# Kernel tuning notes

Hardware: AMD Instinct MI355X
Metric: run time of the kernel (lower is better)

## Reference

```python
import jax, jax.numpy as jnp
import numpy as np

N, D, H, L = 50000, 64, 4, 3
HD = D // H
E = 800000
EPS = 1e-5


def _layernorm(x, g, b):
    m = x.mean(-1, keepdims=True)
    v = ((x - m) ** 2).mean(-1, keepdims=True)
    return (x - m) * jax.lax.rsqrt(v + EPS) * g + b


def setup_inputs() -> dict:
    key = jax.random.key(0)
    ks = jax.random.split(key, 24)
    s = 0.05
    inp = {
        'feats': jax.random.normal(ks[0], (N, D), jnp.float32),
        'edge_index': jax.random.randint(ks[1], (2, E), 0, N, jnp.int64),
        'edge_attr': jax.random.uniform(ks[2], (E,), jnp.float32),
    }
    names = ['Wq', 'Wk', 'Wv', 'Wo', 'W1', 'W2']
    for i, n in enumerate(names):
        inp[n] = jax.random.normal(ks[3 + i], (L, D, D), jnp.float32) * s
    bnames = ['bq', 'bk', 'bv', 'bo', 'b1', 'b2']
    for i, n in enumerate(bnames):
        inp[n] = jnp.zeros((L, D), jnp.float32)
    inp['g1'] = jnp.ones((L, D), jnp.float32)
    inp['be1'] = jnp.zeros((L, D), jnp.float32)
    inp['g2'] = jnp.ones((L, D), jnp.float32)
    inp['be2'] = jnp.zeros((L, D), jnp.float32)
    return inp


def reference(feats, edge_index, edge_attr, Wq, bq, Wk, bk, Wv, bv, Wo, bo,
              W1, b1, W2, b2, g1, be1, g2, be2):
    row, col = edge_index[0], edge_index[1]  # source, destination nodes
    inv_sqrt = 1.0 / np.sqrt(HD).astype(np.float32)
    outs = []
    for l in range(L):
        # multi-head edge-indexed dot-product attention
        q = (feats @ Wq[l] + bq[l]).reshape(N, H, HD)
        k = (feats @ Wk[l] + bk[l]).reshape(N, H, HD)
        v = (feats @ Wv[l] + bv[l]).reshape(N, H, HD)
        scores = (q[col] * k[row]).sum(-1) * inv_sqrt       # [E, H]
        scores = scores * edge_attr[:, None]                # mult_attr modulation
        smax = jax.ops.segment_max(scores, col, num_segments=N)
        alpha = jnp.exp(scores - smax[col])
        denom = jax.ops.segment_sum(alpha, col, num_segments=N)
        alpha = alpha / denom[col]                          # scatter softmax
        agg = jax.ops.segment_sum(alpha[:, :, None] * v[row], col, num_segments=N)
        att = agg.reshape(N, D) @ Wo[l] + bo[l]
        feats = _layernorm(feats + att, g1[l], be1[l])      # res1 + norm1
        mlp = jax.nn.relu(feats @ W1[l] + b1[l]) @ W2[l] + b2[l]
        feats = _layernorm(feats + mlp, g2[l], be2[l])      # res2 + norm2
        outs.append(feats)
    return jnp.stack(outs)  # [L, N, D]
```

## Files before the change

kernel.cpp:

```cpp
#include <hip/hip_runtime.h>

#define NN 50000
#define DIM 64
#define NHEAD 4
#define NEDGE 800000
#define NLAYER 3
#define LN_EPS 1e-5f
#define SCAN_BLOCKS ((NN + 255) / 256)
#define ROWS 8

__device__ __forceinline__ float bcast(float x, int l) {
    return __uint_as_float(__builtin_amdgcn_readlane(__float_as_uint(x), l));
}

__device__ __forceinline__ unsigned int bf16rtn(float x) {
    unsigned int u = __float_as_uint(x);
    return (u + 0x7FFFu + ((u >> 16) & 1u)) >> 16;
}
__device__ __forceinline__ float blo(unsigned int u) {
    return __uint_as_float(u << 16);
}
__device__ __forceinline__ float bhi(unsigned int u) {
    return __uint_as_float(u & 0xFFFF0000u);
}


__global__ __launch_bounds__(256) void zero_kernel(int* __restrict__ p, int n) {
    int i = blockIdx.x * blockDim.x + threadIdx.x;
    if (i < n) p[i] = 0;
}

__global__ __launch_bounds__(256) void deg_kernel(const int* __restrict__ ei,
                                                  int* __restrict__ deg) {
    int e = blockIdx.x * blockDim.x + threadIdx.x;
    if (e < NEDGE) atomicAdd(&deg[ei[NEDGE + e]], 1);
}

__global__ __launch_bounds__(256) void scan1_kernel(const int* __restrict__ deg,
                                                    int* __restrict__ tmp,
                                                    int* __restrict__ bsum) {
    __shared__ int s[256];
    int t = threadIdx.x;
    int i = blockIdx.x * 256 + t;
    int v = (i < NN) ? deg[i] : 0;
    s[t] = v;
    __syncthreads();
    for (int off = 1; off < 256; off <<= 1) {
        int x = (t >= off) ? s[t - off] : 0;
        __syncthreads();
        s[t] += x;
        __syncthreads();
    }
    if (i < NN) tmp[i] = s[t] - v;
    if (t == 255) bsum[blockIdx.x] = s[255];
}

__global__ __launch_bounds__(256) void scan2_kernel(int* __restrict__ bsum) {
    __shared__ int s[256];
    int t = threadIdx.x;
    int v = (t < SCAN_BLOCKS) ? bsum[t] : 0;
    s[t] = v;
    __syncthreads();
    for (int off = 1; off < 256; off <<= 1) {
        int x = (t >= off) ? s[t - off] : 0;
        __syncthreads();
        s[t] += x;
        __syncthreads();
    }
    if (t < SCAN_BLOCKS) bsum[t] = s[t] - v;
}

__global__ __launch_bounds__(256) void scan3_kernel(const int* __restrict__ tmp,
                                                    const int* __restrict__ bsum,
                                                    int* __restrict__ rowptr,
                                                    int* __restrict__ cursor) {
    int i = blockIdx.x * 256 + threadIdx.x;
    if (i < NN) {
        int v = tmp[i] + bsum[i >> 8];
        rowptr[i] = v;
        cursor[i] = v;
    }
    if (i == 0) rowptr[NN] = NEDGE;
}

__global__ __launch_bounds__(256) void fill_kernel(const int* __restrict__ ei,
                                                   const float* __restrict__ attr,
                                                   int* __restrict__ cursor,
                                                   int2* __restrict__ csr) {
    int e = blockIdx.x * blockDim.x + threadIdx.x;
    if (e >= NEDGE) return;
    int src = ei[e];
    int dst = ei[NEDGE + e];
    int idx = atomicAdd(&cursor[dst], 1);
    int2 pk;
    pk.x = src;
    pk.y = __float_as_int(attr[e]);
    csr[idx] = pk;
}


__global__ __launch_bounds__(256) void qkv_kernel(
    const float* __restrict__ feats,
    const float* __restrict__ Wq, const float* __restrict__ Wk, const float* __restrict__ Wv,
    const float* __restrict__ bq, const float* __restrict__ bk, const float* __restrict__ bv,
    float* __restrict__ q, unsigned int* __restrict__ kpk, unsigned int* __restrict__ vpk) {
    int wave = threadIdx.x >> 6;
    int lane = threadIdx.x & 63;
    int n0 = (blockIdx.x * 4 + wave) * ROWS;

    const float* rowp[ROWS];
    float qa[ROWS], ka[ROWS], va[ROWS];
    float biq = bq[lane], bik = bk[lane], biv = bv[lane];
    #pragma unroll
    for (int r = 0; r < ROWS; ++r) {
        int nu = __builtin_amdgcn_readfirstlane(min(n0 + r, NN - 1));
        rowp[r] = feats + (size_t)nu * DIM;
        qa[r] = biq; ka[r] = bik; va[r] = biv;
    }
    #pragma unroll
    for (int kk = 0; kk < DIM; ++kk) {
        float wq = Wq[kk * DIM + lane];
        float wk = Wk[kk * DIM + lane];
        float wv = Wv[kk * DIM + lane];
        #pragma unroll
        for (int r = 0; r < ROWS; ++r) {
            float x = rowp[r][kk];
            qa[r] = fmaf(x, wq, qa[r]);
            ka[r] = fmaf(x, wk, ka[r]);
            va[r] = fmaf(x, wv, va[r]);
        }
    }
    bool evenLane = (lane & 1) == 0;
    #pragma unroll
    for (int r = 0; r < ROWS; ++r) {
        int n = n0 + r;
        if (n < NN) q[n * DIM + lane] = qa[r] * 0.25f;
        unsigned int bk_ = bf16rtn(ka[r]);
        unsigned int bv_ = bf16rtn(va[r]);
        unsigned int nk = __shfl_xor(bk_, 1, 64);
        unsigned int nv = __shfl_xor(bv_, 1, 64);
        if (n < NN && evenLane) {
            kpk[n * 32 + (lane >> 1)] = bk_ | (nk << 16);
            vpk[n * 32 + (lane >> 1)] = bv_ | (nv << 16);
        }
    }
}

__global__ __launch_bounds__(256) void attn_kernel(
    const int* __restrict__ rowptr, const int2* __restrict__ csr,
    const float* __restrict__ q,
    const unsigned int* __restrict__ kpk, const unsigned int* __restrict__ vpk,
    float* __restrict__ agg) {
    int wave = threadIdx.x >> 6;
    int lane = threadIdx.x & 63;
    int quarter = lane >> 4;
    int slot = (lane >> 3) & 1;
    int g = lane & 7;
    int n = blockIdx.x * 16 + wave * 4 + quarter;
    if (n >= NN) return;

    float4 qa = *(const float4*)&q[n * DIM + 8 * g];
    float4 qb = *(const float4*)&q[n * DIM + 8 * g + 4];
    int beg = rowptr[n], end = rowptr[n + 1];

    float denom = 0.f;
    float a0 = 0.f, a1 = 0.f, a2 = 0.f, a3 = 0.f;
    float a4 = 0.f, a5 = 0.f, a6 = 0.f, a7 = 0.f;

    for (int ii = beg + slot; ii < end; ii += 2) {
        int2 me = csr[ii];
        int src = me.x;
        float at = __int_as_float(me.y);
        uint4 ku = *(const uint4*)&kpk[src * 32 + 4 * g];
        uint4 vu = *(const uint4*)&vpk[src * 32 + 4 * g];
        float p = qa.x * blo(ku.x);
        p = fmaf(qa.y, bhi(ku.x), p);
        p = fmaf(qa.z, blo(ku.y), p);
        p = fmaf(qa.w, bhi(ku.y), p);
        p = fmaf(qb.x, blo(ku.z), p);
        p = fmaf(qb.y, bhi(ku.z), p);
        p = fmaf(qb.z, blo(ku.w), p);
        p = fmaf(qb.w, bhi(ku.w), p);
        p += __shfl_xor(p, 1, 64);
        float w = __expf(p * at);
        denom += w;
        a0 = fmaf(w, blo(vu.x), a0);
        a1 = fmaf(w, bhi(vu.x), a1);
        a2 = fmaf(w, blo(vu.y), a2);
        a3 = fmaf(w, bhi(vu.y), a3);
        a4 = fmaf(w, blo(vu.z), a4);
        a5 = fmaf(w, bhi(vu.z), a5);
        a6 = fmaf(w, blo(vu.w), a6);
        a7 = fmaf(w, bhi(vu.w), a7);
    }
    denom += __shfl_xor(denom, 8, 64);
    a0 += __shfl_xor(a0, 8, 64);
    a1 += __shfl_xor(a1, 8, 64);
    a2 += __shfl_xor(a2, 8, 64);
    a3 += __shfl_xor(a3, 8, 64);
    a4 += __shfl_xor(a4, 8, 64);
    a5 += __shfl_xor(a5, 8, 64);
    a6 += __shfl_xor(a6, 8, 64);
    a7 += __shfl_xor(a7, 8, 64);

    if (slot == 0) {
        float inv = (denom > 0.f) ? 1.f / denom : 0.f;
        float4 o1; o1.x = a0 * inv; o1.y = a1 * inv; o1.z = a2 * inv; o1.w = a3 * inv;
        float4 o2; o2.x = a4 * inv; o2.y = a5 * inv; o2.z = a6 * inv; o2.w = a7 * inv;
        *(float4*)&agg[n * DIM + 8 * g] = o1;
        *(float4*)&agg[n * DIM + 8 * g + 4] = o2;
    }
}

__global__ __launch_bounds__(256) void post_kernel(
    const float* __restrict__ feats_in,
    const float* __restrict__ agg,
    const float* __restrict__ Wo, const float* __restrict__ bo,
    const float* __restrict__ W1, const float* __restrict__ b1,
    const float* __restrict__ W2, const float* __restrict__ b2,
    const float* __restrict__ g1, const float* __restrict__ be1,
    const float* __restrict__ g2, const float* __restrict__ be2,
    float* __restrict__ out) {
    int wave = threadIdx.x >> 6;
    int lane = threadIdx.x & 63;
    int n0 = (blockIdx.x * 4 + wave) * ROWS;

    float acc[ROWS], xin[ROWS];
    float bio = bo[lane];
    #pragma unroll
    for (int r = 0; r < ROWS; ++r) {
        int n = min(n0 + r, NN - 1);
        xin[r] = agg[n * DIM + lane];
        acc[r] = bio;
    }
    #pragma unroll
    for (int kk = 0; kk < DIM; ++kk) {
        float w = Wo[kk * DIM + lane];
        #pragma unroll
        for (int r = 0; r < ROWS; ++r)
            acc[r] = fmaf(bcast(xin[r], kk), w, acc[r]);
    }
    float gg1 = g1[lane], bb1 = be1[lane];
    #pragma unroll
    for (int r = 0; r < ROWS; ++r) {
        int n = min(n0 + r, NN - 1);
        float x = feats_in[n * DIM + lane] + acc[r];
        float s1 = x, s2 = x * x;
        #pragma unroll
        for (int o = 32; o >= 1; o >>= 1) {
            s1 += __shfl_xor(s1, o, 64);
            s2 += __shfl_xor(s2, o, 64);
        }
        float mean = s1 * (1.f / 64.f);
        float var = fmaf(-mean, mean, s2 * (1.f / 64.f));
        xin[r] = (x - mean) * rsqrtf(var + LN_EPS) * gg1 + bb1;
    }
    float bi1 = b1[lane];
    #pragma unroll
    for (int r = 0; r < ROWS; ++r) acc[r] = bi1;
    #pragma unroll
    for (int kk = 0; kk < DIM; ++kk) {
        float w = W1[kk * DIM + lane];
        #pragma unroll
        for (int r = 0; r < ROWS; ++r)
            acc[r] = fmaf(bcast(xin[r], kk), w, acc[r]);
    }
    float h[ROWS];
    #pragma unroll
    for (int r = 0; r < ROWS; ++r) h[r] = fmaxf(acc[r], 0.f);
    float bi2 = b2[lane];
    #pragma unroll
    for (int r = 0; r < ROWS; ++r) acc[r] = bi2;
    #pragma unroll
    for (int kk = 0; kk < DIM; ++kk) {
        float w = W2[kk * DIM + lane];
        #pragma unroll
        for (int r = 0; r < ROWS; ++r)
            acc[r] = fmaf(bcast(h[r], kk), w, acc[r]);
    }
    float gg2 = g2[lane], bb2 = be2[lane];
    #pragma unroll
    for (int r = 0; r < ROWS; ++r) {
        int n = n0 + r;
        float x2 = xin[r] + acc[r];
        float s1 = x2, s2 = x2 * x2;
        #pragma unroll
        for (int o = 32; o >= 1; o >>= 1) {
            s1 += __shfl_xor(s1, o, 64);
            s2 += __shfl_xor(s2, o, 64);
        }
        float mean = s1 * (1.f / 64.f);
        float var = fmaf(-mean, mean, s2 * (1.f / 64.f));
        if (n < NN)
            out[n * DIM + lane] = (x2 - mean) * rsqrtf(var + LN_EPS) * gg2 + bb2;
    }
}

extern "C" void kernel_launch(void* const* d_in, const int* in_sizes, int n_in,
                              void* d_out, int out_size, void* d_ws, size_t ws_size,
                              hipStream_t stream) {
    const float* feats = (const float*)d_in[0];
    const int*   ei    = (const int*)d_in[1];
    const float* attr  = (const float*)d_in[2];
    const float* Wq = (const float*)d_in[3];
    const float* Wk = (const float*)d_in[4];
    const float* Wv = (const float*)d_in[5];
    const float* Wo = (const float*)d_in[6];
    const float* W1 = (const float*)d_in[7];
    const float* W2 = (const float*)d_in[8];
    const float* bq = (const float*)d_in[9];
    const float* bk = (const float*)d_in[10];
    const float* bv = (const float*)d_in[11];
    const float* bo = (const float*)d_in[12];
    const float* b1 = (const float*)d_in[13];
    const float* b2 = (const float*)d_in[14];
    const float* g1  = (const float*)d_in[15];
    const float* be1 = (const float*)d_in[16];
    const float* g2  = (const float*)d_in[17];
    const float* be2 = (const float*)d_in[18];

    float* out = (float*)d_out;
    float* ws = (float*)d_ws;

    const size_t ND = (size_t)NN * DIM;
    float* q   = ws;
    float* agg = ws + ND;
    unsigned int* kpk = (unsigned int*)(ws + 2 * ND);
    unsigned int* vpk = kpk + (size_t)NN * 32;

    int* wi = (int*)(vpk + (size_t)NN * 32);
    int* deg      = wi;
    int* cursor   = wi + NN;
    int* tmp      = wi + 2 * NN;
    int* bsum     = wi + 3 * NN;
    int* rowptr   = wi + 3 * NN + 256;
    int2* csr     = (int2*)(rowptr + NN + 2);

    zero_kernel<<<(NN + 255) / 256, 256, 0, stream>>>(deg, NN);
    deg_kernel<<<(NEDGE + 255) / 256, 256, 0, stream>>>(ei, deg);
    scan1_kernel<<<SCAN_BLOCKS, 256, 0, stream>>>(deg, tmp, bsum);
    scan2_kernel<<<1, 256, 0, stream>>>(bsum);
    scan3_kernel<<<SCAN_BLOCKS, 256, 0, stream>>>(tmp, bsum, rowptr, cursor);
    fill_kernel<<<(NEDGE + 255) / 256, 256, 0, stream>>>(ei, attr, cursor, csr);

    const int rowBlocks = (NN + 4 * ROWS - 1) / (4 * ROWS);
    const int attnBlocks = (NN + 15) / 16;
    const float* fin = feats;
    for (int l = 0; l < NLAYER; ++l) {
        const size_t wOff = (size_t)l * DIM * DIM;
        const size_t bOff = (size_t)l * DIM;
        float* lout = out + (size_t)l * ND;

        qkv_kernel<<<rowBlocks, 256, 0, stream>>>(
            fin, Wq + wOff, Wk + wOff, Wv + wOff,
            bq + bOff, bk + bOff, bv + bOff, q, kpk, vpk);

        attn_kernel<<<attnBlocks, 256, 0, stream>>>(rowptr, csr, q, kpk, vpk, agg);

        post_kernel<<<rowBlocks, 256, 0, stream>>>(
            fin, agg,
            Wo + wOff, bo + bOff, W1 + wOff, b1 + bOff, W2 + wOff, b2 + bOff,
            g1 + bOff, be1 + bOff, g2 + bOff, be2 + bOff,
            lout);

        fin = lout;
    }
}
```

Before: 488.2 us.

## Fuse Q projection, edge attention and post-MLP into one kernel; pack CSR entries

The Q projection, the edge-softmax aggregation and the Wo/MLP/LayerNorm stage now run in a single kernel. Q and the aggregated output stay in per-wave LDS instead of making two full N×D global round trips, and one launch per layer is removed. CSR entries shrink from 8 to 4 bytes by packing a 16-bit source index with a bf16 edge attribute, which halves CSR traffic but rounds the edge attribute to bf16 and only works while N fits in 16 bits. Each node is now handled by 8 lanes walking all its edges serially, instead of two interleaved slots, and the attention phase runs with half as many waves. That may reduce latency hiding and load balance in the gather loop.

```diff
diff --git a/kernel.cpp b/kernel.cpp
--- a/kernel.cpp
+++ b/kernel.cpp
@@ -86,46 +86,41 @@
 __global__ __launch_bounds__(256) void fill_kernel(const int* __restrict__ ei,
                                                    const float* __restrict__ attr,
                                                    int* __restrict__ cursor,
-                                                   int2* __restrict__ csr) {
+                                                   unsigned int* __restrict__ csr) {
     int e = blockIdx.x * blockDim.x + threadIdx.x;
     if (e >= NEDGE) return;
     int src = ei[e];
     int dst = ei[NEDGE + e];
     int idx = atomicAdd(&cursor[dst], 1);
-    int2 pk;
-    pk.x = src;
-    pk.y = __float_as_int(attr[e]);
-    csr[idx] = pk;
-}
-
-
-__global__ __launch_bounds__(256) void qkv_kernel(
+    csr[idx] = (unsigned int)src | (bf16rtn(attr[e]) << 16);
+}
+
+
+__global__ __launch_bounds__(256) void kv_kernel(
     const float* __restrict__ feats,
-    const float* __restrict__ Wq, const float* __restrict__ Wk, const float* __restrict__ Wv,
-    const float* __restrict__ bq, const float* __restrict__ bk, const float* __restrict__ bv,
-    float* __restrict__ q, unsigned int* __restrict__ kpk, unsigned int* __restrict__ vpk) {
+    const float* __restrict__ Wk, const float* __restrict__ Wv,
+    const float* __restrict__ bk, const float* __restrict__ bv,
+    unsigned int* __restrict__ kpk, unsigned int* __restrict__ vpk) {
     int wave = threadIdx.x >> 6;
     int lane = threadIdx.x & 63;
     int n0 = (blockIdx.x * 4 + wave) * ROWS;
 
     const float* rowp[ROWS];
-    float qa[ROWS], ka[ROWS], va[ROWS];
-    float biq = bq[lane], bik = bk[lane], biv = bv[lane];
+    float ka[ROWS], va[ROWS];
+    float bik = bk[lane], biv = bv[lane];
     #pragma unroll
     for (int r = 0; r < ROWS; ++r) {
         int nu = __builtin_amdgcn_readfirstlane(min(n0 + r, NN - 1));
         rowp[r] = feats + (size_t)nu * DIM;
-        qa[r] = biq; ka[r] = bik; va[r] = biv;
-    }
-    #pragma unroll
-    for (int kk = 0; kk < DIM; ++kk) {
-        float wq = Wq[kk * DIM + lane];
+        ka[r] = bik; va[r] = biv;
+    }
+    #pragma unroll
+    for (int kk = 0; kk < DIM; ++kk) {
         float wk = Wk[kk * DIM + lane];
         float wv = Wv[kk * DIM + lane];
         #pragma unroll
         for (int r = 0; r < ROWS; ++r) {
             float x = rowp[r][kk];
-            qa[r] = fmaf(x, wq, qa[r]);
             ka[r] = fmaf(x, wk, ka[r]);
             va[r] = fmaf(x, wv, va[r]);
         }
@@ -134,7 +129,6 @@
     #pragma unroll
     for (int r = 0; r < ROWS; ++r) {
         int n = n0 + r;
-        if (n < NN) q[n * DIM + lane] = qa[r] * 0.25f;
         unsigned int bk_ = bf16rtn(ka[r]);
         unsigned int bv_ = bf16rtn(va[r]);
         unsigned int nk = __shfl_xor(bk_, 1, 64);
@@ -146,93 +140,96 @@
     }
 }
 
-__global__ __launch_bounds__(256) void attn_kernel(
-    const int* __restrict__ rowptr, const int2* __restrict__ csr,
-    const float* __restrict__ q,
+__global__ __launch_bounds__(256) void fused_kernel(
+    const float* __restrict__ fin,
+    const float* __restrict__ Wq, const float* __restrict__ bq,
+    const int* __restrict__ rowptr, const unsigned int* __restrict__ csr,
     const unsigned int* __restrict__ kpk, const unsigned int* __restrict__ vpk,
-    float* __restrict__ agg) {
-    int wave = threadIdx.x >> 6;
-    int lane = threadIdx.x & 63;
-    int quarter = lane >> 4;
-    int slot = (lane >> 3) & 1;
-    int g = lane & 7;
-    int n = blockIdx.x * 16 + wave * 4 + quarter;
-    if (n >= NN) return;
-
-    float4 qa = *(const float4*)&q[n * DIM + 8 * g];
-    float4 qb = *(const float4*)&q[n * DIM + 8 * g + 4];
-    int beg = rowptr[n], end = rowptr[n + 1];
-
-    float denom = 0.f;
-    float a0 = 0.f, a1 = 0.f, a2 = 0.f, a3 = 0.f;
-    float a4 = 0.f, a5 = 0.f, a6 = 0.f, a7 = 0.f;
-
-    for (int ii = beg + slot; ii < end; ii += 2) {
-        int2 me = csr[ii];
-        int src = me.x;
-        float at = __int_as_float(me.y);
-        uint4 ku = *(const uint4*)&kpk[src * 32 + 4 * g];
-        uint4 vu = *(const uint4*)&vpk[src * 32 + 4 * g];
-        float p = qa.x * blo(ku.x);
-        p = fmaf(qa.y, bhi(ku.x), p);
-        p = fmaf(qa.z, blo(ku.y), p);
-        p = fmaf(qa.w, bhi(ku.y), p);
-        p = fmaf(qb.x, blo(ku.z), p);
-        p = fmaf(qb.y, bhi(ku.z), p);
-        p = fmaf(qb.z, blo(ku.w), p);
-        p = fmaf(qb.w, bhi(ku.w), p);
-        p += __shfl_xor(p, 1, 64);
-        float w = __expf(p * at);
-        denom += w;
-        a0 = fmaf(w, blo(vu.x), a0);
-        a1 = fmaf(w, bhi(vu.x), a1);
-        a2 = fmaf(w, blo(vu.y), a2);
-        a3 = fmaf(w, bhi(vu.y), a3);
-        a4 = fmaf(w, blo(vu.z), a4);
-        a5 = fmaf(w, bhi(vu.z), a5);
-        a6 = fmaf(w, blo(vu.w), a6);
-        a7 = fmaf(w, bhi(vu.w), a7);
-    }
-    denom += __shfl_xor(denom, 8, 64);
-    a0 += __shfl_xor(a0, 8, 64);
-    a1 += __shfl_xor(a1, 8, 64);
-    a2 += __shfl_xor(a2, 8, 64);
-    a3 += __shfl_xor(a3, 8, 64);
-    a4 += __shfl_xor(a4, 8, 64);
-    a5 += __shfl_xor(a5, 8, 64);
-    a6 += __shfl_xor(a6, 8, 64);
-    a7 += __shfl_xor(a7, 8, 64);
-
-    if (slot == 0) {
-        float inv = (denom > 0.f) ? 1.f / denom : 0.f;
-        float4 o1; o1.x = a0 * inv; o1.y = a1 * inv; o1.z = a2 * inv; o1.w = a3 * inv;
-        float4 o2; o2.x = a4 * inv; o2.y = a5 * inv; o2.z = a6 * inv; o2.w = a7 * inv;
-        *(float4*)&agg[n * DIM + 8 * g] = o1;
-        *(float4*)&agg[n * DIM + 8 * g + 4] = o2;
-    }
-}
-
-__global__ __launch_bounds__(256) void post_kernel(
-    const float* __restrict__ feats_in,
-    const float* __restrict__ agg,
     const float* __restrict__ Wo, const float* __restrict__ bo,
     const float* __restrict__ W1, const float* __restrict__ b1,
     const float* __restrict__ W2, const float* __restrict__ b2,
     const float* __restrict__ g1, const float* __restrict__ be1,
     const float* __restrict__ g2, const float* __restrict__ be2,
     float* __restrict__ out) {
+    __shared__ float sh[4 * ROWS * DIM];
     int wave = threadIdx.x >> 6;
     int lane = threadIdx.x & 63;
+    float* lds = &sh[wave * ROWS * DIM];
     int n0 = (blockIdx.x * 4 + wave) * ROWS;
 
-    float acc[ROWS], xin[ROWS];
+    const float* rowp[ROWS];
+    float acc[ROWS];
+    float biq = bq[lane];
+    #pragma unroll
+    for (int r = 0; r < ROWS; ++r) {
+        int nu = __builtin_amdgcn_readfirstlane(min(n0 + r, NN - 1));
+        rowp[r] = fin + (size_t)nu * DIM;
+        acc[r] = biq;
+    }
+    #pragma unroll
+    for (int kk = 0; kk < DIM; ++kk) {
+        float wq = Wq[kk * DIM + lane];
+        #pragma unroll
+        for (int r = 0; r < ROWS; ++r)
+            acc[r] = fmaf(rowp[r][kk], wq, acc[r]);
+    }
+    #pragma unroll
+    for (int r = 0; r < ROWS; ++r) lds[r * DIM + lane] = acc[r] * 0.25f;
+
+    {
+        int grp = lane >> 3;
+        int g = lane & 7;
+        int n = n0 + grp;
+        bool act = n < NN;
+        int nc = min(n, NN - 1);
+        float4 qa = *(const float4*)&lds[grp * DIM + 8 * g];
+        float4 qb = *(const float4*)&lds[grp * DIM + 8 * g + 4];
+        int beg = rowptr[nc];
+        int end = act ? rowptr[nc + 1] : beg;
+
+        float denom = 0.f;
+        float a0 = 0.f, a1 = 0.f, a2 = 0.f, a3 = 0.f;
+        float a4 = 0.f, a5 = 0.f, a6 = 0.f, a7 = 0.f;
+        for (int ii = beg; ii < end; ++ii) {
+            unsigned int me = csr[ii];
+            int src = (int)(me & 0xFFFFu);
+            float at = bhi(me);
+            uint4 ku = *(const uint4*)&kpk[src * 32 + 4 * g];
+            uint4 vu = *(const uint4*)&vpk[src * 32 + 4 * g];
+            float p = qa.x * blo(ku.x);
+            p = fmaf(qa.y, bhi(ku.x), p);
+            p = fmaf(qa.z, blo(ku.y), p);
+            p = fmaf(qa.w, bhi(ku.y), p);
+            p = fmaf(qb.x, blo(ku.z), p);
+            p = fmaf(qb.y, bhi(ku.z), p);
+            p = fmaf(qb.z, blo(ku.w), p);
+            p = fmaf(qb.w, bhi(ku.w), p);
+            p += __shfl_xor(p, 1, 64);
+            float w = __expf(p * at);
+            denom += w;
+            a0 = fmaf(w, blo(vu.x), a0);
+            a1 = fmaf(w, bhi(vu.x), a1);
+            a2 = fmaf(w, blo(vu.y), a2);
+            a3 = fmaf(w, bhi(vu.y), a3);
+            a4 = fmaf(w, blo(vu.z), a4);
+            a5 = fmaf(w, bhi(vu.z), a5);
+            a6 = fmaf(w, blo(vu.w), a6);
+            a7 = fmaf(w, bhi(vu.w), a7);
+        }
+        float inv = (denom > 0.f) ? 1.f / denom : 0.f;
+        float4 o1; o1.x = a0 * inv; o1.y = a1 * inv; o1.z = a2 * inv; o1.w = a3 * inv;
+        float4 o2; o2.x = a4 * inv; o2.y = a5 * inv; o2.z = a6 * inv; o2.w = a7 * inv;
+        *(float4*)&lds[grp * DIM + 8 * g] = o1;
+        *(float4*)&lds[grp * DIM + 8 * g + 4] = o2;
+    }
+
+    float xin[ROWS];
+    #pragma unroll
+    for (int r = 0; r < ROWS; ++r) xin[r] = lds[r * DIM + lane];
+
     float bio = bo[lane];
     #pragma unroll
-    for (int r = 0; r < ROWS; ++r) {
-        int n = min(n0 + r, NN - 1);
-        xin[r] = agg[n * DIM + lane];
-        acc[r] = bio;
-    }
+    for (int r = 0; r < ROWS; ++r) acc[r] = bio;
     #pragma unroll
     for (int kk = 0; kk < DIM; ++kk) {
         float w = Wo[kk * DIM + lane];
@@ -244,7 +241,7 @@
     #pragma unroll
     for (int r = 0; r < ROWS; ++r) {
         int n = min(n0 + r, NN - 1);
-        float x = feats_in[n * DIM + lane] + acc[r];
+        float x = fin[(size_t)n * DIM + lane] + acc[r];
         float s1 = x, s2 = x * x;
         #pragma unroll
         for (int o = 32; o >= 1; o >>= 1) {
@@ -292,7 +289,7 @@
         float mean = s1 * (1.f / 64.f);
         float var = fmaf(-mean, mean, s2 * (1.f / 64.f));
         if (n < NN)
-            out[n * DIM + lane] = (x2 - mean) * rsqrtf(var + LN_EPS) * gg2 + bb2;
+            out[(size_t)n * DIM + lane] = (x2 - mean) * rsqrtf(var + LN_EPS) * gg2 + bb2;
     }
 }
 
@@ -322,10 +319,7 @@
     float* out = (float*)d_out;
     float* ws = (float*)d_ws;
 
-    const size_t ND = (size_t)NN * DIM;
-    float* q   = ws;
-    float* agg = ws + ND;
-    unsigned int* kpk = (unsigned int*)(ws + 2 * ND);
+    unsigned int* kpk = (unsigned int*)ws;
     unsigned int* vpk = kpk + (size_t)NN * 32;
 
     int* wi = (int*)(vpk + (size_t)NN * 32);
@@ -334,7 +328,7 @@
     int* tmp      = wi + 2 * NN;
     int* bsum     = wi + 3 * NN;
     int* rowptr   = wi + 3 * NN + 256;
-    int2* csr     = (int2*)(rowptr + NN + 2);
+    unsigned int* csr = (unsigned int*)(rowptr + NN + 1);
 
     zero_kernel<<<(NN + 255) / 256, 256, 0, stream>>>(deg, NN);
     deg_kernel<<<(NEDGE + 255) / 256, 256, 0, stream>>>(ei, deg);
@@ -344,21 +338,17 @@
     fill_kernel<<<(NEDGE + 255) / 256, 256, 0, stream>>>(ei, attr, cursor, csr);
 
     const int rowBlocks = (NN + 4 * ROWS - 1) / (4 * ROWS);
-    const int attnBlocks = (NN + 15) / 16;
     const float* fin = feats;
     for (int l = 0; l < NLAYER; ++l) {
         const size_t wOff = (size_t)l * DIM * DIM;
         const size_t bOff = (size_t)l * DIM;
-        float* lout = out + (size_t)l * ND;
-
-        qkv_kernel<<<rowBlocks, 256, 0, stream>>>(
-            fin, Wq + wOff, Wk + wOff, Wv + wOff,
-            bq + bOff, bk + bOff, bv + bOff, q, kpk, vpk);
-
-        attn_kernel<<<attnBlocks, 256, 0, stream>>>(rowptr, csr, q, kpk, vpk, agg);
-
-        post_kernel<<<rowBlocks, 256, 0, stream>>>(
-            fin, agg,
+        float* lout = out + (size_t)l * NN * DIM;
+
+        kv_kernel<<<rowBlocks, 256, 0, stream>>>(
+            fin, Wk + wOff, Wv + wOff, bk + bOff, bv + bOff, kpk, vpk);
+
+        fused_kernel<<<rowBlocks, 256, 0, stream>>>(
+            fin, Wq + wOff, bq + bOff, rowptr, csr, kpk, vpk,
             Wo + wOff, bo + bOff, W1 + wOff, b1 + bOff, W2 + wOff, b2 + bOff,
             g1 + bOff, be1 + bOff, g2 + bOff, be2 + bOff,
             lout);
```

New measurement: 568.5 us. 1.16x slower.
